# Performance work log

Measured on AMD Instinct MI355X. Metric: run time of the kernel, lower is better.

Reference implementation:

```python
import jax, jax.numpy as jnp
import numpy as np

N = 262144          # anchors
NUM_CLASSES = 80
DET_DIM = 4 + NUM_CLASSES
TOP_K = 1000
MAX_BOXES = 300
NMS_THRESHOLD = 0.4


def setup_inputs() -> dict:
    key = jax.random.key(0)
    k1, k2, k3, k4, k5 = jax.random.split(key, 5)
    # boxes in (x1, y1, x2, y2) format with x2 > x1, y2 > y1
    xy1 = jax.random.uniform(k1, (1, N, 2), dtype=jnp.float32) * 1000.0
    wh = jax.random.uniform(k2, (1, N, 2), dtype=jnp.float32) * 100.0 + 1.0
    boxes = jnp.concatenate([xy1, xy1 + wh], axis=-1)              # [1, N, 4]
    classification = jax.random.uniform(k3, (1, N, NUM_CLASSES), dtype=jnp.float32)
    detections = jax.random.normal(k4, (1, N, DET_DIM), dtype=jnp.float32)
    return {"boxes": boxes, "classification": classification, "detections": detections}


def _iou_matrix(b):
    # b: [K, 4] in (x1, y1, x2, y2)
    x1, y1, x2, y2 = b[:, 0], b[:, 1], b[:, 2], b[:, 3]
    area = (x2 - x1) * (y2 - y1)
    ix1 = jnp.maximum(x1[:, None], x1[None, :])
    iy1 = jnp.maximum(y1[:, None], y1[None, :])
    ix2 = jnp.minimum(x2[:, None], x2[None, :])
    iy2 = jnp.minimum(y2[:, None], y2[None, :])
    inter = jnp.maximum(ix2 - ix1, 0.0) * jnp.maximum(iy2 - iy1, 0.0)
    union = area[:, None] + area[None, :] - inter
    return inter / jnp.maximum(union, 1e-8)


def _nms(boxes, scores, iou_threshold, max_output_size):
    # Greedy NMS (tf.image.non_max_suppression semantics) on K boxes.
    K = boxes.shape[0]
    order = jnp.argsort(-scores)              # descending score
    iou = _iou_matrix(boxes[order])           # [K, K] in sorted order
    ar = jnp.arange(K)

    def body(suppressed, i):
        active = jnp.logical_not(suppressed[i])
        suppressed = suppressed | (active & (iou[i] > iou_threshold) & (ar > i))
        return suppressed, active

    _, keep = jax.lax.scan(body, jnp.zeros((K,), jnp.bool_), ar)
    # fixed-size selection of kept positions (in score order), padded with K
    sel = jnp.nonzero(keep, size=max_output_size, fill_value=K)[0]
    valid = sel < K
    order_pad = jnp.concatenate([order, jnp.zeros((1,), order.dtype)])
    return order_pad[sel], valid


def reference(boxes, classification, detections):
    b = boxes[0]                               # [N, 4]
    c = classification[0]                      # [N, C]
    d = detections[0]                          # [N, D]
    scores = jnp.max(c, axis=1)                # per-anchor best class score
    scores_k, idx_k = jax.lax.top_k(scores, TOP_K)
    b_k = b[idx_k]                             # [TOP_K, 4]
    d_k = d[idx_k]                             # [TOP_K, D]
    nms_idx, valid = _nms(b_k, scores_k, NMS_THRESHOLD, MAX_BOXES)
    # original returns a ragged [1, n_kept, D]; we return fixed [1, MAX_BOXES, D]
    # with invalid rows zeroed (padding for jit-compatibility)
    out = d_k[nms_idx] * valid[:, None].astype(d_k.dtype)
    return out[None]                           # [1, MAX_BOXES, D]
```

## Files before the change

kernel.cpp:

```cpp
#include <hip/hip_runtime.h>
#include <stdint.h>

#define N_ANCH 262144
#define NUM_CLASSES 80
#define DET_DIM 84
#define TOP_K 1000
#define MAX_BOXES 300
#define NMS_THR 0.4f

#define OFF_KEYS   0u
#define OFF_HIST1  (N_ANCH * 4u)
#define OFF_HIST2  (OFF_HIST1 + 16384u)
#define OFF_HIST3  (OFF_HIST2 + 16384u)
#define OFF_STATE  (OFF_HIST3 + 1024u)
#define OFF_LISTA  (OFF_STATE + 64u)
#define OFF_LISTB  (OFF_LISTA + 4096u)
#define OFF_TOPK   (OFF_LISTB + 16384u)
#define OFF_BOXK   (OFF_TOPK + 4096u)
#define OFF_MASK   (OFF_BOXK + 16384u)
#define OFF_SEL    (OFF_MASK + 131072u)

#define ZERO_WORDS ((16384u + 16384u + 1024u + 64u) / 4u)

__global__ __launch_bounds__(256) void k_init(uint32_t* __restrict__ z) {
    uint32_t tid = blockIdx.x * 256u + threadIdx.x;
    if (tid < ZERO_WORDS) z[tid] = 0u;
}

__global__ __launch_bounds__(256) void k_scores(const float* __restrict__ cls,
                                                uint32_t* __restrict__ keys,
                                                uint32_t* __restrict__ ghist1) {
    __shared__ uint32_t h[4096];
    for (int i = threadIdx.x; i < 4096; i += 256) h[i] = 0u;
    __syncthreads();
    int stride = gridDim.x * 256;
    for (int a = blockIdx.x * 256 + threadIdx.x; a < N_ANCH; a += stride) {
        const float4* q = (const float4*)(cls + (size_t)a * NUM_CLASSES);
        float m = -1.0f;
#pragma unroll
        for (int t = 0; t < 20; ++t) {
            float4 v = q[t];
            m = fmaxf(m, fmaxf(fmaxf(v.x, v.y), fmaxf(v.z, v.w)));
        }
        uint32_t key = __float_as_uint(m);
        keys[a] = key;
        atomicAdd(&h[key >> 20], 1u);
    }
    __syncthreads();
    for (int i = threadIdx.x; i < 4096; i += 256) {
        uint32_t v = h[i];
        if (v) atomicAdd(&ghist1[i], v);
    }
}

__device__ __forceinline__ void wave_scan_hist(const uint32_t* __restrict__ hist,
                                               int nbins, uint32_t k,
                                               uint32_t* __restrict__ out, int lane) {
    int per = nbins >> 6;
    int base = lane * per;
    uint32_t partial = 0;
    for (int b = 0; b < per; ++b) partial += hist[base + b];
    uint32_t si = partial;
#pragma unroll
    for (int off = 1; off < 64; off <<= 1) {
        uint32_t v = __shfl_down(si, off);
        if (lane + off < 64) si += v;
    }
    uint32_t se = si - partial;
    if (se < k && k <= si) {
        uint32_t running = se;
        for (int b = base + per - 1; b >= base; --b) {
            uint32_t hv = hist[b];
            running += hv;
            if (running >= k) {
                out[0] = (uint32_t)b;
                out[1] = k - (running - hv);
                break;
            }
        }
    }
}

__global__ __launch_bounds__(256) void k_pass2(const uint32_t* __restrict__ keys,
                                               const uint32_t* __restrict__ ghist1,
                                               uint32_t* __restrict__ ghist2,
                                               uint32_t* __restrict__ state) {
    __shared__ uint32_t sd[2];
    __shared__ uint32_t h[4096];
    if (threadIdx.x < 64) wave_scan_hist(ghist1, 4096, TOP_K, sd, threadIdx.x);
    for (int i = threadIdx.x; i < 4096; i += 256) h[i] = 0u;
    __syncthreads();
    uint32_t d1 = sd[0], k1 = sd[1];
    if (threadIdx.x == 0 && blockIdx.x == 0) { state[0] = d1; state[1] = k1; }
    int stride = gridDim.x * 256;
    for (int a = blockIdx.x * 256 + threadIdx.x; a < N_ANCH; a += stride) {
        uint32_t key = keys[a];
        if ((key >> 20) == d1) atomicAdd(&h[(key >> 8) & 0xFFFu], 1u);
    }
    __syncthreads();
    for (int i = threadIdx.x; i < 4096; i += 256) {
        uint32_t v = h[i];
        if (v) atomicAdd(&ghist2[i], v);
    }
}

__global__ __launch_bounds__(256) void k_pass3(const uint32_t* __restrict__ keys,
                                               const uint32_t* __restrict__ ghist2,
                                               uint32_t* __restrict__ ghist3,
                                               uint32_t* __restrict__ state) {
    __shared__ uint32_t sd[2];
    if (threadIdx.x < 64) {
        uint32_t k1 = state[1];
        wave_scan_hist(ghist2, 4096, k1, sd, threadIdx.x);
    }
    __syncthreads();
    uint32_t pre24 = (state[0] << 12) | sd[0];
    uint32_t k2 = sd[1];
    if (threadIdx.x == 0 && blockIdx.x == 0) { state[2] = pre24; state[3] = k2; }
    int stride = gridDim.x * 256;
    for (int a = blockIdx.x * 256 + threadIdx.x; a < N_ANCH; a += stride) {
        uint32_t key = keys[a];
        if ((key >> 8) == pre24) atomicAdd(&ghist3[key & 0xFFu], 1u);
    }
}

__global__ __launch_bounds__(256) void k_compact(const uint32_t* __restrict__ keys,
                                                 const uint32_t* __restrict__ ghist3,
                                                 uint32_t* __restrict__ state,
                                                 uint32_t* __restrict__ listA,
                                                 uint32_t* __restrict__ listB) {
    __shared__ uint32_t sd[2];
    if (threadIdx.x < 64) {
        uint32_t k2 = state[3];
        wave_scan_hist(ghist3, 256, k2, sd, threadIdx.x);
    }
    __syncthreads();
    uint32_t T = (state[2] << 8) | sd[0];
    if (threadIdx.x == 0 && blockIdx.x == 0) { state[4] = T; state[5] = sd[1]; }
    int stride = gridDim.x * 256;
    for (int a = blockIdx.x * 256 + threadIdx.x; a < N_ANCH; a += stride) {
        uint32_t key = keys[a];
        if (key > T) {
            uint32_t p = atomicAdd(&state[6], 1u);
            if (p < 1024u) listA[p] = (uint32_t)a;
        } else if (key == T) {
            uint32_t p = atomicAdd(&state[7], 1u);
            if (p < 4096u) listB[p] = (uint32_t)a;
        }
    }
}

__global__ __launch_bounds__(1024) void k_finalize(const uint32_t* __restrict__ keys,
                                                   const uint32_t* __restrict__ state,
                                                   const uint32_t* __restrict__ listA,
                                                   const uint32_t* __restrict__ listB,
                                                   uint32_t* __restrict__ topk,
                                                   const float4* __restrict__ boxes,
                                                   float4* __restrict__ boxk) {
    __shared__ unsigned long long A[1024];
    __shared__ uint32_t Bv[4096];
    __shared__ uint32_t tk[1000];
    int t = threadIdx.x;
    uint32_t cntA = state[6]; if (cntA > 999u) cntA = 999u;
    uint32_t cntB = state[7]; if (cntB > 4096u) cntB = 4096u;
    uint32_t r = TOP_K - cntA;

    unsigned long long wv = ~0ull;
    if (t < (int)cntA) {
        uint32_t idx = listA[t];
        uint32_t key = keys[idx];
        wv = ((unsigned long long)(key ^ 0xFFFFFFFFu) << 32) | (unsigned long long)idx;
    }
    A[t] = wv;
    __syncthreads();
    unsigned n2 = 1; while (n2 < cntA) n2 <<= 1;
    for (unsigned k = 2; k <= n2; k <<= 1) {
        for (unsigned j = k >> 1; j > 0; j >>= 1) {
            unsigned i = (unsigned)t;
            unsigned ixj = i ^ j;
            if (i < n2 && ixj > i) {
                unsigned long long a = A[i], b = A[ixj];
                bool up = ((i & k) == 0);
                if (up ? (a > b) : (a < b)) { A[i] = b; A[ixj] = a; }
            }
            __syncthreads();
        }
    }
    if (t < (int)cntA) tk[t] = (uint32_t)(A[t] & 0xFFFFFFFFull);

    unsigned n2b = 1; while (n2b < cntB) n2b <<= 1;
    for (unsigned i = (unsigned)t; i < n2b; i += 1024) Bv[i] = (i < cntB) ? listB[i] : 0xFFFFFFFFu;
    __syncthreads();
    for (unsigned k = 2; k <= n2b; k <<= 1) {
        for (unsigned j = k >> 1; j > 0; j >>= 1) {
            for (unsigned i = (unsigned)t; i < n2b; i += 1024) {
                unsigned ixj = i ^ j;
                if (ixj > i) {
                    uint32_t a = Bv[i], b = Bv[ixj];
                    bool up = ((i & k) == 0);
                    if (up ? (a > b) : (a < b)) { Bv[i] = b; Bv[ixj] = a; }
                }
            }
            __syncthreads();
        }
    }
    if (t < (int)r) tk[cntA + t] = Bv[t];
    __syncthreads();
    if (t < 1000) {
        uint32_t idx = tk[t];
        topk[t] = idx;
        boxk[t] = boxes[idx];
    }
}

__global__ __launch_bounds__(256) void k_mask(const float4* __restrict__ boxk,
                                              unsigned long long* __restrict__ mask) {
    __shared__ float4 bx[1000];
    for (int i = threadIdx.x; i < 1000; i += 256) bx[i] = boxk[i];
    __syncthreads();
    int i = blockIdx.x;
    if (i >= 1000) {
        if (threadIdx.x < 16) mask[(size_t)i * 16 + threadIdx.x] = 0ull;
        return;
    }
    float4 bi = bx[i];
    float areai = __fmul_rn(__fsub_rn(bi.z, bi.x), __fsub_rn(bi.w, bi.y));
    int lane = threadIdx.x & 63;
    int wave = threadIdx.x >> 6;
#pragma unroll
    for (int rr = 0; rr < 4; ++rr) {
        int j = rr * 256 + threadIdx.x;
        bool bit = false;
        if (j < 1000 && j > i) {
            float4 bj = bx[j];
            float areaj = __fmul_rn(__fsub_rn(bj.z, bj.x), __fsub_rn(bj.w, bj.y));
            float ix1 = fmaxf(bi.x, bj.x);
            float iy1 = fmaxf(bi.y, bj.y);
            float ix2 = fminf(bi.z, bj.z);
            float iy2 = fminf(bi.w, bj.w);
            float iw = fmaxf(__fsub_rn(ix2, ix1), 0.0f);
            float ih = fmaxf(__fsub_rn(iy2, iy1), 0.0f);
            float inter = __fmul_rn(iw, ih);
            float uni = __fsub_rn(__fadd_rn(areai, areaj), inter);
            float den = fmaxf(uni, 1e-8f);
            float iou = inter / den;
            bit = iou > NMS_THR;
        }
        unsigned long long bal = __ballot(bit);
        if (lane == 0) mask[(size_t)i * 16 + (rr * 4 + wave)] = bal;
    }
}

__global__ __launch_bounds__(64) void k_nms(const unsigned long long* __restrict__ mask,
                                            const uint32_t* __restrict__ topk,
                                            uint32_t* __restrict__ sel) {
    __shared__ uint32_t keptList[384];
    int lane = threadIdx.x;
    uint32_t keptCount = 0;
    for (int c = 0; c < 16; ++c) {
        unsigned long long acc = 0ull;
        for (uint32_t s = (uint32_t)lane; s < keptCount; s += 64u)
            acc |= mask[(size_t)keptList[s] * 16 + c];
#pragma unroll
        for (int off = 1; off < 64; off <<= 1) acc |= __shfl_xor(acc, off);
        unsigned long long supp = acc;
        unsigned long long row = mask[(size_t)(c * 64 + lane) * 16 + c];
        for (int i = 0; i < 64; ++i) {
            unsigned long long ri = __shfl(row, i);
            if (!((supp >> i) & 1ull)) supp |= ri;
        }
        unsigned long long validm = (c == 15) ? ((1ull << 40) - 1ull) : ~0ull;
        unsigned long long kept = (~supp) & validm;
        uint32_t cnt = (uint32_t)__popcll(kept);
        if ((kept >> lane) & 1ull) {
            uint32_t pos = keptCount + (uint32_t)__popcll(kept & ((1ull << lane) - 1ull));
            if (pos < 384u) keptList[pos] = (uint32_t)(c * 64 + lane);
        }
        keptCount += cnt;
        __syncthreads();
        if (keptCount >= MAX_BOXES) break;
    }
    for (uint32_t m = (uint32_t)lane; m < MAX_BOXES; m += 64u)
        sel[m] = (m < keptCount) ? topk[keptList[m]] : 0xFFFFFFFFu;
}

__global__ __launch_bounds__(256) void k_out(const uint32_t* __restrict__ sel,
                                             const float* __restrict__ det,
                                             float* __restrict__ out) {
    int tid = blockIdx.x * 256 + threadIdx.x;
    if (tid >= MAX_BOXES * DET_DIM) return;
    int m = tid / DET_DIM;
    int e = tid - m * DET_DIM;
    uint32_t s = sel[m];
    out[tid] = (s == 0xFFFFFFFFu) ? 0.0f : det[(size_t)s * DET_DIM + e];
}

extern "C" void kernel_launch(void* const* d_in, const int* in_sizes, int n_in,
                              void* d_out, int out_size, void* d_ws, size_t ws_size,
                              hipStream_t stream) {
    const float* boxes = (const float*)d_in[0];
    const float* cls   = (const float*)d_in[1];
    const float* det   = (const float*)d_in[2];
    float* out = (float*)d_out;
    char* ws = (char*)d_ws;

    uint32_t* keys  = (uint32_t*)(ws + OFF_KEYS);
    uint32_t* h1    = (uint32_t*)(ws + OFF_HIST1);
    uint32_t* h2    = (uint32_t*)(ws + OFF_HIST2);
    uint32_t* h3    = (uint32_t*)(ws + OFF_HIST3);
    uint32_t* st    = (uint32_t*)(ws + OFF_STATE);
    uint32_t* listA = (uint32_t*)(ws + OFF_LISTA);
    uint32_t* listB = (uint32_t*)(ws + OFF_LISTB);
    uint32_t* topk  = (uint32_t*)(ws + OFF_TOPK);
    float4*   boxk  = (float4*)(ws + OFF_BOXK);
    unsigned long long* mask = (unsigned long long*)(ws + OFF_MASK);
    uint32_t* sel   = (uint32_t*)(ws + OFF_SEL);

    k_init<<<dim3((ZERO_WORDS + 255) / 256), dim3(256), 0, stream>>>(h1);
    k_scores<<<dim3(512), dim3(256), 0, stream>>>(cls, keys, h1);
    k_pass2<<<dim3(256), dim3(256), 0, stream>>>(keys, h1, h2, st);
    k_pass3<<<dim3(256), dim3(256), 0, stream>>>(keys, h2, h3, st);
    k_compact<<<dim3(256), dim3(256), 0, stream>>>(keys, h3, st, listA, listB);
    k_finalize<<<dim3(1), dim3(1024), 0, stream>>>(keys, st, listA, listB, topk,
                                                   (const float4*)boxes, boxk);
    k_mask<<<dim3(1024), dim3(256), 0, stream>>>(boxk, mask);
    k_nms<<<dim3(1), dim3(64), 0, stream>>>(mask, topk, sel);
    k_out<<<dim3((MAX_BOXES * DET_DIM + 255) / 256), dim3(256), 0, stream>>>(sel, det, out);
}
```

Baseline: 243.6 us.

## Fuse selection and NMS stages into cooperative kernels; quad-split score reduction

Merges the three radix-select passes and compaction into one cooperative kernel, separated by grid-wide syncs. Merges top-k finalize, IoU mask, greedy NMS and output gather into a second cooperative kernel, cutting the launch sequence from nine kernels to four and removing the inter-kernel gaps and state round-trips. The class-score max kernel now gives each anchor to four lanes, which read interleaved float4s and combine them with shuffles, so each load instruction touches neighbouring memory. In exchange it relies on cooperative launch residency, and it adds grid-sync costs while the serial single-block phases leave most of the grid idle.

```diff
diff --git a/kernel.cpp b/kernel.cpp
--- a/kernel.cpp
+++ b/kernel.cpp
@@ -1,5 +1,8 @@
 #include <hip/hip_runtime.h>
+#include <hip/hip_cooperative_groups.h>
 #include <stdint.h>
+
+namespace cg = cooperative_groups;
 
 #define N_ANCH 262144
 #define NUM_CLASSES 80
@@ -33,18 +36,23 @@
     __shared__ uint32_t h[4096];
     for (int i = threadIdx.x; i < 4096; i += 256) h[i] = 0u;
     __syncthreads();
-    int stride = gridDim.x * 256;
-    for (int a = blockIdx.x * 256 + threadIdx.x; a < N_ANCH; a += stride) {
-        const float4* q = (const float4*)(cls + (size_t)a * NUM_CLASSES);
+    int q = threadIdx.x & 3;
+    int stride = gridDim.x * 64;
+    for (int a = blockIdx.x * 64 + (threadIdx.x >> 2); a < N_ANCH; a += stride) {
+        const float4* p = (const float4*)(cls + (size_t)a * NUM_CLASSES) + q;
         float m = -1.0f;
 #pragma unroll
-        for (int t = 0; t < 20; ++t) {
-            float4 v = q[t];
+        for (int t = 0; t < 5; ++t) {
+            float4 v = p[4 * t];
             m = fmaxf(m, fmaxf(fmaxf(v.x, v.y), fmaxf(v.z, v.w)));
         }
-        uint32_t key = __float_as_uint(m);
-        keys[a] = key;
-        atomicAdd(&h[key >> 20], 1u);
+        m = fmaxf(m, __shfl_xor(m, 1));
+        m = fmaxf(m, __shfl_xor(m, 2));
+        if (q == 0) {
+            uint32_t key = __float_as_uint(m);
+            keys[a] = key;
+            atomicAdd(&h[key >> 20], 1u);
+        }
     }
     __syncthreads();
     for (int i = threadIdx.x; i < 4096; i += 256) {
@@ -81,18 +89,22 @@
     }
 }
 
-__global__ __launch_bounds__(256) void k_pass2(const uint32_t* __restrict__ keys,
-                                               const uint32_t* __restrict__ ghist1,
-                                               uint32_t* __restrict__ ghist2,
-                                               uint32_t* __restrict__ state) {
+__global__ __launch_bounds__(256) void k_select(const uint32_t* __restrict__ keys,
+                                                const uint32_t* __restrict__ gh1,
+                                                uint32_t* __restrict__ gh2,
+                                                uint32_t* __restrict__ gh3,
+                                                uint32_t* __restrict__ state,
+                                                uint32_t* __restrict__ listA,
+                                                uint32_t* __restrict__ listB) {
+    cg::grid_group grid = cg::this_grid();
     __shared__ uint32_t sd[2];
     __shared__ uint32_t h[4096];
-    if (threadIdx.x < 64) wave_scan_hist(ghist1, 4096, TOP_K, sd, threadIdx.x);
+    int stride = gridDim.x * 256;
+
+    if (threadIdx.x < 64) wave_scan_hist(gh1, 4096, TOP_K, sd, threadIdx.x);
     for (int i = threadIdx.x; i < 4096; i += 256) h[i] = 0u;
     __syncthreads();
     uint32_t d1 = sd[0], k1 = sd[1];
-    if (threadIdx.x == 0 && blockIdx.x == 0) { state[0] = d1; state[1] = k1; }
-    int stride = gridDim.x * 256;
     for (int a = blockIdx.x * 256 + threadIdx.x; a < N_ANCH; a += stride) {
         uint32_t key = keys[a];
         if ((key >> 20) == d1) atomicAdd(&h[(key >> 8) & 0xFFFu], 1u);
@@ -100,44 +112,23 @@
     __syncthreads();
     for (int i = threadIdx.x; i < 4096; i += 256) {
         uint32_t v = h[i];
-        if (v) atomicAdd(&ghist2[i], v);
-    }
-}
-
-__global__ __launch_bounds__(256) void k_pass3(const uint32_t* __restrict__ keys,
-                                               const uint32_t* __restrict__ ghist2,
-                                               uint32_t* __restrict__ ghist3,
-                                               uint32_t* __restrict__ state) {
-    __shared__ uint32_t sd[2];
-    if (threadIdx.x < 64) {
-        uint32_t k1 = state[1];
-        wave_scan_hist(ghist2, 4096, k1, sd, threadIdx.x);
-    }
-    __syncthreads();
-    uint32_t pre24 = (state[0] << 12) | sd[0];
+        if (v) atomicAdd(&gh2[i], v);
+    }
+    grid.sync();
+
+    if (threadIdx.x < 64) wave_scan_hist(gh2, 4096, k1, sd, threadIdx.x);
+    __syncthreads();
+    uint32_t pre24 = (d1 << 12) | sd[0];
     uint32_t k2 = sd[1];
-    if (threadIdx.x == 0 && blockIdx.x == 0) { state[2] = pre24; state[3] = k2; }
-    int stride = gridDim.x * 256;
     for (int a = blockIdx.x * 256 + threadIdx.x; a < N_ANCH; a += stride) {
         uint32_t key = keys[a];
-        if ((key >> 8) == pre24) atomicAdd(&ghist3[key & 0xFFu], 1u);
-    }
-}
-
-__global__ __launch_bounds__(256) void k_compact(const uint32_t* __restrict__ keys,
-                                                 const uint32_t* __restrict__ ghist3,
-                                                 uint32_t* __restrict__ state,
-                                                 uint32_t* __restrict__ listA,
-                                                 uint32_t* __restrict__ listB) {
-    __shared__ uint32_t sd[2];
-    if (threadIdx.x < 64) {
-        uint32_t k2 = state[3];
-        wave_scan_hist(ghist3, 256, k2, sd, threadIdx.x);
-    }
-    __syncthreads();
-    uint32_t T = (state[2] << 8) | sd[0];
-    if (threadIdx.x == 0 && blockIdx.x == 0) { state[4] = T; state[5] = sd[1]; }
-    int stride = gridDim.x * 256;
+        if ((key >> 8) == pre24) atomicAdd(&gh3[key & 0xFFu], 1u);
+    }
+    grid.sync();
+
+    if (threadIdx.x < 64) wave_scan_hist(gh3, 256, k2, sd, threadIdx.x);
+    __syncthreads();
+    uint32_t T = (pre24 << 8) | sd[0];
     for (int a = blockIdx.x * 256 + threadIdx.x; a < N_ANCH; a += stride) {
         uint32_t key = keys[a];
         if (key > T) {
@@ -150,88 +141,92 @@
     }
 }
 
-__global__ __launch_bounds__(1024) void k_finalize(const uint32_t* __restrict__ keys,
-                                                   const uint32_t* __restrict__ state,
-                                                   const uint32_t* __restrict__ listA,
-                                                   const uint32_t* __restrict__ listB,
-                                                   uint32_t* __restrict__ topk,
-                                                   const float4* __restrict__ boxes,
-                                                   float4* __restrict__ boxk) {
+__global__ __launch_bounds__(1024) void k_final(const uint32_t* __restrict__ keys,
+                                                const uint32_t* __restrict__ state,
+                                                const uint32_t* __restrict__ listA,
+                                                const uint32_t* __restrict__ listB,
+                                                uint32_t* __restrict__ topk,
+                                                const float4* __restrict__ boxes,
+                                                float4* __restrict__ boxk,
+                                                unsigned long long* __restrict__ mask,
+                                                uint32_t* __restrict__ sel,
+                                                const float* __restrict__ det,
+                                                float* __restrict__ out) {
+    cg::grid_group grid = cg::this_grid();
     __shared__ unsigned long long A[1024];
     __shared__ uint32_t Bv[4096];
     __shared__ uint32_t tk[1000];
+    __shared__ float4 bx[1000];
+    __shared__ uint32_t keptList[384];
+    __shared__ uint32_t sKept;
     int t = threadIdx.x;
-    uint32_t cntA = state[6]; if (cntA > 999u) cntA = 999u;
-    uint32_t cntB = state[7]; if (cntB > 4096u) cntB = 4096u;
-    uint32_t r = TOP_K - cntA;
-
-    unsigned long long wv = ~0ull;
-    if (t < (int)cntA) {
-        uint32_t idx = listA[t];
-        uint32_t key = keys[idx];
-        wv = ((unsigned long long)(key ^ 0xFFFFFFFFu) << 32) | (unsigned long long)idx;
-    }
-    A[t] = wv;
-    __syncthreads();
-    unsigned n2 = 1; while (n2 < cntA) n2 <<= 1;
-    for (unsigned k = 2; k <= n2; k <<= 1) {
-        for (unsigned j = k >> 1; j > 0; j >>= 1) {
-            unsigned i = (unsigned)t;
-            unsigned ixj = i ^ j;
-            if (i < n2 && ixj > i) {
-                unsigned long long a = A[i], b = A[ixj];
-                bool up = ((i & k) == 0);
-                if (up ? (a > b) : (a < b)) { A[i] = b; A[ixj] = a; }
+
+    if (blockIdx.x == 0) {
+        uint32_t cntA = state[6]; if (cntA > 999u) cntA = 999u;
+        uint32_t cntB = state[7]; if (cntB > 4096u) cntB = 4096u;
+        uint32_t r = TOP_K - cntA;
+
+        unsigned long long wv = ~0ull;
+        if (t < (int)cntA) {
+            uint32_t idx = listA[t];
+            uint32_t key = keys[idx];
+            wv = ((unsigned long long)(key ^ 0xFFFFFFFFu) << 32) | (unsigned long long)idx;
+        }
+        A[t] = wv;
+        __syncthreads();
+        unsigned n2 = 1; while (n2 < cntA) n2 <<= 1;
+        for (unsigned k = 2; k <= n2; k <<= 1) {
+            for (unsigned j = k >> 1; j > 0; j >>= 1) {
+                unsigned i = (unsigned)t;
+                unsigned ixj = i ^ j;
+                if (i < n2 && ixj > i) {
+                    unsigned long long a = A[i], b = A[ixj];
+                    bool up = ((i & k) == 0);
+                    if (up ? (a > b) : (a < b)) { A[i] = b; A[ixj] = a; }
+                }
+                __syncthreads();
             }
-            __syncthreads();
-        }
-    }
-    if (t < (int)cntA) tk[t] = (uint32_t)(A[t] & 0xFFFFFFFFull);
-
-    unsigned n2b = 1; while (n2b < cntB) n2b <<= 1;
-    for (unsigned i = (unsigned)t; i < n2b; i += 1024) Bv[i] = (i < cntB) ? listB[i] : 0xFFFFFFFFu;
-    __syncthreads();
-    for (unsigned k = 2; k <= n2b; k <<= 1) {
-        for (unsigned j = k >> 1; j > 0; j >>= 1) {
-            for (unsigned i = (unsigned)t; i < n2b; i += 1024) {
-                unsigned ixj = i ^ j;
-                if (ixj > i) {
-                    uint32_t a = Bv[i], b = Bv[ixj];
-                    bool up = ((i & k) == 0);
-                    if (up ? (a > b) : (a < b)) { Bv[i] = b; Bv[ixj] = a; }
+        }
+        if (t < (int)cntA) tk[t] = (uint32_t)(A[t] & 0xFFFFFFFFull);
+
+        unsigned n2b = 1; while (n2b < cntB) n2b <<= 1;
+        for (unsigned i = (unsigned)t; i < n2b; i += 1024) Bv[i] = (i < cntB) ? listB[i] : 0xFFFFFFFFu;
+        __syncthreads();
+        for (unsigned k = 2; k <= n2b; k <<= 1) {
+            for (unsigned j = k >> 1; j > 0; j >>= 1) {
+                for (unsigned i = (unsigned)t; i < n2b; i += 1024) {
+                    unsigned ixj = i ^ j;
+                    if (ixj > i) {
+                        uint32_t a = Bv[i], b = Bv[ixj];
+                        bool up = ((i & k) == 0);
+                        if (up ? (a > b) : (a < b)) { Bv[i] = b; Bv[ixj] = a; }
+                    }
                 }
+                __syncthreads();
             }
-            __syncthreads();
-        }
-    }
-    if (t < (int)r) tk[cntA + t] = Bv[t];
-    __syncthreads();
-    if (t < 1000) {
-        uint32_t idx = tk[t];
-        topk[t] = idx;
-        boxk[t] = boxes[idx];
-    }
-}
-
-__global__ __launch_bounds__(256) void k_mask(const float4* __restrict__ boxk,
-                                              unsigned long long* __restrict__ mask) {
-    __shared__ float4 bx[1000];
-    for (int i = threadIdx.x; i < 1000; i += 256) bx[i] = boxk[i];
-    __syncthreads();
-    int i = blockIdx.x;
-    if (i >= 1000) {
-        if (threadIdx.x < 16) mask[(size_t)i * 16 + threadIdx.x] = 0ull;
-        return;
-    }
-    float4 bi = bx[i];
-    float areai = __fmul_rn(__fsub_rn(bi.z, bi.x), __fsub_rn(bi.w, bi.y));
-    int lane = threadIdx.x & 63;
-    int wave = threadIdx.x >> 6;
-#pragma unroll
-    for (int rr = 0; rr < 4; ++rr) {
-        int j = rr * 256 + threadIdx.x;
+        }
+        if (t < (int)r) tk[cntA + t] = Bv[t];
+        __syncthreads();
+        if (t < 1000) {
+            uint32_t idx = tk[t];
+            topk[t] = idx;
+            boxk[t] = boxes[idx];
+        }
+    }
+    grid.sync();
+
+    for (int i = t; i < 1000; i += 1024) bx[i] = boxk[i];
+    __syncthreads();
+    for (int r = blockIdx.x; r < 1024; r += gridDim.x) {
+        if (r >= 1000) {
+            if (t < 16) mask[(size_t)r * 16 + t] = 0ull;
+            continue;
+        }
+        float4 bi = bx[r];
+        float areai = __fmul_rn(__fsub_rn(bi.z, bi.x), __fsub_rn(bi.w, bi.y));
         bool bit = false;
-        if (j < 1000 && j > i) {
+        int j = t;
+        if (j < 1000 && j > r) {
             float4 bj = bx[j];
             float areaj = __fmul_rn(__fsub_rn(bj.z, bj.x), __fsub_rn(bj.w, bj.y));
             float ix1 = fmaxf(bi.x, bj.x);
@@ -247,52 +242,55 @@
             bit = iou > NMS_THR;
         }
         unsigned long long bal = __ballot(bit);
-        if (lane == 0) mask[(size_t)i * 16 + (rr * 4 + wave)] = bal;
-    }
-}
-
-__global__ __launch_bounds__(64) void k_nms(const unsigned long long* __restrict__ mask,
-                                            const uint32_t* __restrict__ topk,
-                                            uint32_t* __restrict__ sel) {
-    __shared__ uint32_t keptList[384];
-    int lane = threadIdx.x;
-    uint32_t keptCount = 0;
-    for (int c = 0; c < 16; ++c) {
-        unsigned long long acc = 0ull;
-        for (uint32_t s = (uint32_t)lane; s < keptCount; s += 64u)
-            acc |= mask[(size_t)keptList[s] * 16 + c];
+        if ((t & 63) == 0) mask[(size_t)r * 16 + (t >> 6)] = bal;
+    }
+    grid.sync();
+
+    if (blockIdx.x == 0) {
+        int lane = t & 63;
+        int wv0 = t >> 6;
+        uint32_t keptCount = 0;
+        uint32_t kc = 0;
+        for (int c = 0; c < 16; ++c) {
+            if (wv0 == 0) {
+                unsigned long long acc = 0ull;
+                for (uint32_t s = (uint32_t)lane; s < keptCount; s += 64u)
+                    acc |= mask[(size_t)keptList[s] * 16 + c];
 #pragma unroll
-        for (int off = 1; off < 64; off <<= 1) acc |= __shfl_xor(acc, off);
-        unsigned long long supp = acc;
-        unsigned long long row = mask[(size_t)(c * 64 + lane) * 16 + c];
-        for (int i = 0; i < 64; ++i) {
-            unsigned long long ri = __shfl(row, i);
-            if (!((supp >> i) & 1ull)) supp |= ri;
-        }
-        unsigned long long validm = (c == 15) ? ((1ull << 40) - 1ull) : ~0ull;
-        unsigned long long kept = (~supp) & validm;
-        uint32_t cnt = (uint32_t)__popcll(kept);
-        if ((kept >> lane) & 1ull) {
-            uint32_t pos = keptCount + (uint32_t)__popcll(kept & ((1ull << lane) - 1ull));
-            if (pos < 384u) keptList[pos] = (uint32_t)(c * 64 + lane);
-        }
-        keptCount += cnt;
-        __syncthreads();
-        if (keptCount >= MAX_BOXES) break;
-    }
-    for (uint32_t m = (uint32_t)lane; m < MAX_BOXES; m += 64u)
-        sel[m] = (m < keptCount) ? topk[keptList[m]] : 0xFFFFFFFFu;
-}
-
-__global__ __launch_bounds__(256) void k_out(const uint32_t* __restrict__ sel,
-                                             const float* __restrict__ det,
-                                             float* __restrict__ out) {
-    int tid = blockIdx.x * 256 + threadIdx.x;
-    if (tid >= MAX_BOXES * DET_DIM) return;
-    int m = tid / DET_DIM;
-    int e = tid - m * DET_DIM;
-    uint32_t s = sel[m];
-    out[tid] = (s == 0xFFFFFFFFu) ? 0.0f : det[(size_t)s * DET_DIM + e];
+                for (int off = 1; off < 64; off <<= 1) acc |= __shfl_xor(acc, off);
+                unsigned long long supp = acc;
+                unsigned long long row = mask[(size_t)(c * 64 + lane) * 16 + c];
+                for (int i = 0; i < 64; ++i) {
+                    unsigned long long ri = __shfl(row, i);
+                    if (!((supp >> i) & 1ull)) supp |= ri;
+                }
+                unsigned long long validm = (c == 15) ? ((1ull << 40) - 1ull) : ~0ull;
+                unsigned long long kept = (~supp) & validm;
+                uint32_t cnt = (uint32_t)__popcll(kept);
+                if ((kept >> lane) & 1ull) {
+                    uint32_t pos = keptCount + (uint32_t)__popcll(kept & ((1ull << lane) - 1ull));
+                    if (pos < 384u) keptList[pos] = (uint32_t)(c * 64 + lane);
+                }
+                keptCount += cnt;
+                if (lane == 0) sKept = keptCount;
+            }
+            __syncthreads();
+            kc = sKept;
+            __syncthreads();
+            if (kc >= MAX_BOXES) break;
+        }
+        for (uint32_t m = (uint32_t)t; m < MAX_BOXES; m += 1024u)
+            sel[m] = (m < kc) ? topk[keptList[m]] : 0xFFFFFFFFu;
+    }
+    grid.sync();
+
+    int g = blockIdx.x * 1024 + t;
+    if (g < MAX_BOXES * DET_DIM) {
+        int m = g / DET_DIM;
+        int e = g - m * DET_DIM;
+        uint32_t s = sel[m];
+        out[g] = (s == 0xFFFFFFFFu) ? 0.0f : det[(size_t)s * DET_DIM + e];
+    }
 }
 
 extern "C" void kernel_launch(void* const* d_in, const int* in_sizes, int n_in,
@@ -318,12 +316,18 @@
 
     k_init<<<dim3((ZERO_WORDS + 255) / 256), dim3(256), 0, stream>>>(h1);
     k_scores<<<dim3(512), dim3(256), 0, stream>>>(cls, keys, h1);
-    k_pass2<<<dim3(256), dim3(256), 0, stream>>>(keys, h1, h2, st);
-    k_pass3<<<dim3(256), dim3(256), 0, stream>>>(keys, h2, h3, st);
-    k_compact<<<dim3(256), dim3(256), 0, stream>>>(keys, h3, st, listA, listB);
-    k_finalize<<<dim3(1), dim3(1024), 0, stream>>>(keys, st, listA, listB, topk,
-                                                   (const float4*)boxes, boxk);
-    k_mask<<<dim3(1024), dim3(256), 0, stream>>>(boxk, mask);
-    k_nms<<<dim3(1), dim3(64), 0, stream>>>(mask, topk, sel);
-    k_out<<<dim3((MAX_BOXES * DET_DIM + 255) / 256), dim3(256), 0, stream>>>(sel, det, out);
-}
+
+    {
+        void* args[] = { (void*)&keys, (void*)&h1, (void*)&h2, (void*)&h3,
+                         (void*)&st, (void*)&listA, (void*)&listB };
+        hipLaunchCooperativeKernel((const void*)k_select, dim3(256), dim3(256),
+                                   args, 0, stream);
+    }
+    {
+        void* args[] = { (void*)&keys, (void*)&st, (void*)&listA, (void*)&listB,
+                         (void*)&topk, (void*)&boxes, (void*)&boxk, (void*)&mask,
+                         (void*)&sel, (void*)&det, (void*)&out };
+        hipLaunchCooperativeKernel((const void*)k_final, dim3(256), dim3(1024),
+                                   args, 0, stream);
+    }
+}
```

Result: slower. 369.4 us (+51.6%).

## Replace single-block bitonic sort with parallel rank sort and coalesce score reads

Applied to the files above, without the earlier changes.

The single 1024-thread block that bitonic-sorted the above-threshold and tie candidate lists is replaced by a 16-block rank kernel. Each element counts how many elements outrank it and scatters itself to that position, which removes the many barrier-separated sort stages. The score kernel now uses four lanes per anchor with strided float4 loads and shuffle reductions, so class-row reads are better coalesced. Box gathering moves into the mask kernel, which drops the boxk intermediate. The rank approach costs quadratic compares per list, and the tie-list loop reads listB from global memory.

```diff
diff --git a/kernel.cpp b/kernel.cpp
--- a/kernel.cpp
+++ b/kernel.cpp
@@ -33,18 +33,23 @@
     __shared__ uint32_t h[4096];
     for (int i = threadIdx.x; i < 4096; i += 256) h[i] = 0u;
     __syncthreads();
-    int stride = gridDim.x * 256;
-    for (int a = blockIdx.x * 256 + threadIdx.x; a < N_ANCH; a += stride) {
-        const float4* q = (const float4*)(cls + (size_t)a * NUM_CLASSES);
+    int q = threadIdx.x & 3;
+    int stride = gridDim.x * 64;
+    for (int a = blockIdx.x * 64 + (threadIdx.x >> 2); a < N_ANCH; a += stride) {
+        const float4* p = (const float4*)(cls + (size_t)a * NUM_CLASSES) + q;
         float m = -1.0f;
 #pragma unroll
-        for (int t = 0; t < 20; ++t) {
-            float4 v = q[t];
+        for (int t = 0; t < 5; ++t) {
+            float4 v = p[4 * t];
             m = fmaxf(m, fmaxf(fmaxf(v.x, v.y), fmaxf(v.z, v.w)));
         }
-        uint32_t key = __float_as_uint(m);
-        keys[a] = key;
-        atomicAdd(&h[key >> 20], 1u);
+        m = fmaxf(m, __shfl_xor(m, 1));
+        m = fmaxf(m, __shfl_xor(m, 2));
+        if (q == 0) {
+            uint32_t key = __float_as_uint(m);
+            keys[a] = key;
+            atomicAdd(&h[key >> 20], 1u);
+        }
     }
     __syncthreads();
     for (int i = threadIdx.x; i < 4096; i += 256) {
@@ -150,73 +155,46 @@
     }
 }
 
-__global__ __launch_bounds__(1024) void k_finalize(const uint32_t* __restrict__ keys,
-                                                   const uint32_t* __restrict__ state,
-                                                   const uint32_t* __restrict__ listA,
-                                                   const uint32_t* __restrict__ listB,
-                                                   uint32_t* __restrict__ topk,
-                                                   const float4* __restrict__ boxes,
-                                                   float4* __restrict__ boxk) {
-    __shared__ unsigned long long A[1024];
-    __shared__ uint32_t Bv[4096];
-    __shared__ uint32_t tk[1000];
-    int t = threadIdx.x;
+__global__ __launch_bounds__(256) void k_rank(const uint32_t* __restrict__ keys,
+                                              const uint32_t* __restrict__ state,
+                                              const uint32_t* __restrict__ listA,
+                                              const uint32_t* __restrict__ listB,
+                                              uint32_t* __restrict__ topk) {
+    __shared__ uint32_t kA[1024];
+    __shared__ uint32_t iA[1024];
     uint32_t cntA = state[6]; if (cntA > 999u) cntA = 999u;
     uint32_t cntB = state[7]; if (cntB > 4096u) cntB = 4096u;
     uint32_t r = TOP_K - cntA;
-
-    unsigned long long wv = ~0ull;
+    for (int i = threadIdx.x; i < (int)cntA; i += 256) {
+        uint32_t idx = listA[i];
+        iA[i] = idx;
+        kA[i] = keys[idx];
+    }
+    __syncthreads();
+    int t = blockIdx.x * 256 + threadIdx.x;
     if (t < (int)cntA) {
-        uint32_t idx = listA[t];
-        uint32_t key = keys[idx];
-        wv = ((unsigned long long)(key ^ 0xFFFFFFFFu) << 32) | (unsigned long long)idx;
-    }
-    A[t] = wv;
-    __syncthreads();
-    unsigned n2 = 1; while (n2 < cntA) n2 <<= 1;
-    for (unsigned k = 2; k <= n2; k <<= 1) {
-        for (unsigned j = k >> 1; j > 0; j >>= 1) {
-            unsigned i = (unsigned)t;
-            unsigned ixj = i ^ j;
-            if (i < n2 && ixj > i) {
-                unsigned long long a = A[i], b = A[ixj];
-                bool up = ((i & k) == 0);
-                if (up ? (a > b) : (a < b)) { A[i] = b; A[ixj] = a; }
-            }
-            __syncthreads();
-        }
-    }
-    if (t < (int)cntA) tk[t] = (uint32_t)(A[t] & 0xFFFFFFFFull);
-
-    unsigned n2b = 1; while (n2b < cntB) n2b <<= 1;
-    for (unsigned i = (unsigned)t; i < n2b; i += 1024) Bv[i] = (i < cntB) ? listB[i] : 0xFFFFFFFFu;
-    __syncthreads();
-    for (unsigned k = 2; k <= n2b; k <<= 1) {
-        for (unsigned j = k >> 1; j > 0; j >>= 1) {
-            for (unsigned i = (unsigned)t; i < n2b; i += 1024) {
-                unsigned ixj = i ^ j;
-                if (ixj > i) {
-                    uint32_t a = Bv[i], b = Bv[ixj];
-                    bool up = ((i & k) == 0);
-                    if (up ? (a > b) : (a < b)) { Bv[i] = b; Bv[ixj] = a; }
-                }
-            }
-            __syncthreads();
-        }
-    }
-    if (t < (int)r) tk[cntA + t] = Bv[t];
-    __syncthreads();
-    if (t < 1000) {
-        uint32_t idx = tk[t];
-        topk[t] = idx;
-        boxk[t] = boxes[idx];
-    }
-}
-
-__global__ __launch_bounds__(256) void k_mask(const float4* __restrict__ boxk,
+        uint32_t myk = kA[t], myi = iA[t];
+        uint32_t rank = 0;
+        for (uint32_t j = 0; j < cntA; ++j) {
+            uint32_t kj = kA[j];
+            rank += (kj > myk) || (kj == myk && iA[j] < myi);
+        }
+        topk[rank] = myi;
+    }
+    if (t < (int)cntB) {
+        uint32_t myi = listB[t];
+        uint32_t rank = 0;
+        for (uint32_t j = 0; j < cntB; ++j)
+            rank += (listB[j] < myi);
+        if (rank < r) topk[cntA + rank] = myi;
+    }
+}
+
+__global__ __launch_bounds__(256) void k_mask(const uint32_t* __restrict__ topk,
+                                              const float4* __restrict__ boxes,
                                               unsigned long long* __restrict__ mask) {
     __shared__ float4 bx[1000];
-    for (int i = threadIdx.x; i < 1000; i += 256) bx[i] = boxk[i];
+    for (int i = threadIdx.x; i < 1000; i += 256) bx[i] = boxes[topk[i]];
     __syncthreads();
     int i = blockIdx.x;
     if (i >= 1000) {
@@ -312,7 +290,6 @@
     uint32_t* listA = (uint32_t*)(ws + OFF_LISTA);
     uint32_t* listB = (uint32_t*)(ws + OFF_LISTB);
     uint32_t* topk  = (uint32_t*)(ws + OFF_TOPK);
-    float4*   boxk  = (float4*)(ws + OFF_BOXK);
     unsigned long long* mask = (unsigned long long*)(ws + OFF_MASK);
     uint32_t* sel   = (uint32_t*)(ws + OFF_SEL);
 
@@ -321,9 +298,8 @@
     k_pass2<<<dim3(256), dim3(256), 0, stream>>>(keys, h1, h2, st);
     k_pass3<<<dim3(256), dim3(256), 0, stream>>>(keys, h2, h3, st);
     k_compact<<<dim3(256), dim3(256), 0, stream>>>(keys, h3, st, listA, listB);
-    k_finalize<<<dim3(1), dim3(1024), 0, stream>>>(keys, st, listA, listB, topk,
-                                                   (const float4*)boxes, boxk);
-    k_mask<<<dim3(1024), dim3(256), 0, stream>>>(boxk, mask);
+    k_rank<<<dim3(16), dim3(256), 0, stream>>>(keys, st, listA, listB, topk);
+    k_mask<<<dim3(1024), dim3(256), 0, stream>>>(topk, (const float4*)boxes, mask);
     k_nms<<<dim3(1), dim3(64), 0, stream>>>(mask, topk, sel);
     k_out<<<dim3((MAX_BOXES * DET_DIM + 255) / 256), dim3(256), 0, stream>>>(sel, det, out);
 }
```

Result: slower. 248.8 us (+2.1%).
